# Kernel optimization log

Measured on AMD Instinct MI355X. Metric: run time of the kernel, lower is better.

## Reference

```python
import jax, jax.numpy as jnp
import numpy as np

TEMPERATURE = 8.0  # sqrt(head_dim=64)
NEG_INF = -1000000000.0


def setup_inputs() -> dict:
    key = jax.random.key(0)
    kq, kk, kv, km = jax.random.split(key, 4)
    B, H, S, D = 2, 16, 2048, 64
    q = jax.random.normal(kq, (B, H, S, D), dtype=jnp.float32)
    k = jax.random.normal(kk, (B, H, S, D), dtype=jnp.float32)
    v = jax.random.normal(kv, (B, H, S, D), dtype=jnp.float32)
    mask = jax.random.randint(km, (B, 1, S, S), 0, 2, dtype=jnp.int32)
    return {"q": q, "k": k, "v": v, "mask": mask}


def reference(q, k, v, mask):
    # scores: [B,H,S,S] = (q/T) @ k^T
    attn = jnp.einsum('bhqd,bhkd->bhqk', q / TEMPERATURE, k)
    attn = jnp.where(mask == 0, NEG_INF, attn)
    attn = jax.nn.softmax(attn, axis=-1)  # dropout is identity in eval mode
    output = jnp.einsum('bhqk,bhkd->bhqd', attn, v)
    return (output, attn)
```

## Files before the change

kernel.cpp:

```cpp
#include <hip/hip_runtime.h>
#include <hip/hip_bf16.h>


using short4v = __attribute__((ext_vector_type(4))) short;
using short8v = __attribute__((ext_vector_type(8))) short;
using float4v = __attribute__((ext_vector_type(4))) float;

#define S_LEN 2048
#define D_DIM 64
#define QT 64
#define KTILE 64
#define NIT (S_LEN / KTILE)
#define LDK 72
#define ATTN_OFF (2 * 16 * 2048 * 64)

__device__ __forceinline__ short f2bf(float x) {
  __hip_bfloat16 h = __float2bfloat16(x);
  return __builtin_bit_cast(short, h);
}

__global__ __launch_bounds__(256) void sdpa_kernel(
    const float* __restrict__ q, const float* __restrict__ k,
    const float* __restrict__ v, const int* __restrict__ mask,
    float* __restrict__ out) {
  __shared__ short lds_k[KTILE * LDK];
  __shared__ short lds_vt[D_DIM * LDK];
  __shared__ short lds_p[4 * 16 * LDK];
  __shared__ unsigned short lds_mb[NIT * 256];

  const int tid  = threadIdx.x;
  const int wave = tid >> 6;
  const int lane = tid & 63;
  const int quad = lane >> 4;
  const int l16  = lane & 15;

  const int blk = blockIdx.x;
  const int qt  = blk & (NIT - 1);
  const int bh  = blk >> 5;
  const int b   = bh >> 4;

  const float* qp = q + (size_t)bh * S_LEN * D_DIM;
  const float* kp = k + (size_t)bh * S_LEN * D_DIM;
  const float* vp = v + (size_t)bh * S_LEN * D_DIM;
  const int*   mp = mask + (size_t)b * S_LEN * S_LEN;
  float* outO = out + (size_t)bh * S_LEN * D_DIM;
  float* outA = out + (size_t)ATTN_OFF + (size_t)bh * S_LEN * S_LEN;

  const int qbase = qt * QT;

  const float QSCALE = 0.18033688011112042f;
  short8v qa[2];
  {
    const int qrow = qbase + wave * 16 + l16;
    const float* src = qp + (size_t)qrow * D_DIM + quad * 8;
#pragma unroll
    for (int c = 0; c < 2; ++c) {
      float4v x0 = *(const float4v*)(src + c * 32);
      float4v x1 = *(const float4v*)(src + c * 32 + 4);
      short8v t;
      t[0] = f2bf(x0[0] * QSCALE); t[1] = f2bf(x0[1] * QSCALE);
      t[2] = f2bf(x0[2] * QSCALE); t[3] = f2bf(x0[3] * QSCALE);
      t[4] = f2bf(x1[0] * QSCALE); t[5] = f2bf(x1[1] * QSCALE);
      t[6] = f2bf(x1[2] * QSCALE); t[7] = f2bf(x1[3] * QSCALE);
      qa[c] = t;
    }
  }

  float lsum[4] = {0.f, 0.f, 0.f, 0.f};

#pragma unroll 1
  for (int kt = 0; kt < NIT; ++kt) {
#pragma unroll
    for (int i = 0; i < 4; ++i) {
      int f = tid + i * 256;
      int row = f >> 4;
      int col = (f & 15) * 4;
      float4v x = *(const float4v*)(kp + (size_t)(kt * KTILE + row) * D_DIM + col);
      short4v y;
      y[0] = f2bf(x[0]); y[1] = f2bf(x[1]); y[2] = f2bf(x[2]); y[3] = f2bf(x[3]);
      *(short4v*)(lds_k + row * LDK + col) = y;
    }
    __syncthreads();

    unsigned mb = 0;
    const int qrowC = qbase + wave * 16 + quad * 4;
#pragma unroll
    for (int t = 0; t < 4; ++t) {
      float4v acc = {0.f, 0.f, 0.f, 0.f};
#pragma unroll
      for (int c = 0; c < 2; ++c) {
        short8v bf = *(const short8v*)(lds_k + (t * 16 + l16) * LDK + c * 32 + quad * 8);
        acc = __builtin_amdgcn_mfma_f32_16x16x32_bf16(qa[c], bf, acc, 0, 0, 0);
      }
      const int kcol = kt * KTILE + t * 16 + l16;
      const int* mrow = mp + (size_t)qrowC * S_LEN + kcol;
#pragma unroll
      for (int r = 0; r < 4; ++r) {
        int mv = mrow[(size_t)r * S_LEN];
        float p = mv ? exp2f(acc[r]) : 0.f;
        lsum[r] += p;
        mb |= (mv ? 1u : 0u) << (t * 4 + r);
      }
    }
    lds_mb[kt * 256 + tid] = (unsigned short)mb;
    __syncthreads();
  }

  float invl[4];
#pragma unroll
  for (int r = 0; r < 4; ++r) {
    float s = lsum[r];
    s += __shfl_xor(s, 1);
    s += __shfl_xor(s, 2);
    s += __shfl_xor(s, 4);
    s += __shfl_xor(s, 8);
    invl[r] = 1.0f / s;
  }

  float4v oacc[4];
#pragma unroll
  for (int dt = 0; dt < 4; ++dt) oacc[dt] = (float4v){0.f, 0.f, 0.f, 0.f};

#pragma unroll 1
  for (int kt = 0; kt < NIT; ++kt) {
#pragma unroll
    for (int i = 0; i < 4; ++i) {
      int f = tid + i * 256;
      int row = f >> 4;
      int col = (f & 15) * 4;
      float4v x = *(const float4v*)(kp + (size_t)(kt * KTILE + row) * D_DIM + col);
      short4v y;
      y[0] = f2bf(x[0]); y[1] = f2bf(x[1]); y[2] = f2bf(x[2]); y[3] = f2bf(x[3]);
      *(short4v*)(lds_k + row * LDK + col) = y;
    }
    {
      const int d = tid & 63;
      const int krg = (tid >> 6) * 4;
#pragma unroll
      for (int i = 0; i < 4; ++i) {
        int kr0 = i * 16 + krg;
        short4v y;
#pragma unroll
        for (int j = 0; j < 4; ++j) {
          float x = vp[(size_t)(kt * KTILE + kr0 + j) * D_DIM + d];
          y[j] = f2bf(x);
        }
        *(short4v*)(lds_vt + d * LDK + kr0) = y;
      }
    }
    __syncthreads();

    const unsigned mb = lds_mb[kt * 256 + tid];
    const int qrowC = qbase + wave * 16 + quad * 4;
#pragma unroll
    for (int t = 0; t < 4; ++t) {
      float4v acc = {0.f, 0.f, 0.f, 0.f};
#pragma unroll
      for (int c = 0; c < 2; ++c) {
        short8v bf = *(const short8v*)(lds_k + (t * 16 + l16) * LDK + c * 32 + quad * 8);
        acc = __builtin_amdgcn_mfma_f32_16x16x32_bf16(qa[c], bf, acc, 0, 0, 0);
      }
      const int kcol = kt * KTILE + t * 16 + l16;
      float* arow = outA + (size_t)qrowC * S_LEN + kcol;
      short* prow = lds_p + (wave * 16 + quad * 4) * LDK + t * 16 + l16;
#pragma unroll
      for (int r = 0; r < 4; ++r) {
        float p = ((mb >> (t * 4 + r)) & 1u) ? exp2f(acc[r]) * invl[r] : 0.f;
        arow[(size_t)r * S_LEN] = p;
        prow[r * LDK] = f2bf(p);
      }
    }
#pragma unroll
    for (int c = 0; c < 2; ++c) {
      short8v pa = *(const short8v*)(lds_p + (wave * 16 + l16) * LDK + c * 32 + quad * 8);
#pragma unroll
      for (int dt = 0; dt < 4; ++dt) {
        short8v vb = *(const short8v*)(lds_vt + (dt * 16 + l16) * LDK + c * 32 + quad * 8);
        oacc[dt] = __builtin_amdgcn_mfma_f32_16x16x32_bf16(pa, vb, oacc[dt], 0, 0, 0);
      }
    }
    __syncthreads();
  }

  {
    const int qrowC = qbase + wave * 16 + quad * 4;
    float* orow = outO + (size_t)qrowC * D_DIM + l16;
#pragma unroll
    for (int dt = 0; dt < 4; ++dt) {
#pragma unroll
      for (int r = 0; r < 4; ++r) {
        orow[(size_t)r * D_DIM + dt * 16] = oacc[dt][r];
      }
    }
  }
}

extern "C" void kernel_launch(void* const* d_in, const int* in_sizes, int n_in,
                              void* d_out, int out_size, void* d_ws, size_t ws_size,
                              hipStream_t stream) {
  const float* q = (const float*)d_in[0];
  const float* k = (const float*)d_in[1];
  const float* v = (const float*)d_in[2];
  const int* mask = (const int*)d_in[3];
  float* out = (float*)d_out;

  const int BH = 2 * 16;
  dim3 grid(BH * (S_LEN / QT));
  dim3 block(256);
  sdpa_kernel<<<grid, block, 0, stream>>>(q, k, v, mask, out);
}
```

Measured before the change: 1.014 ms.

## Pack mask into bitmask words and write attention rows through LDS

Adds a pre-pass kernel that compresses the int32 mask into 64-bit ballot words in the workspace. The attention kernel then reads one word per row per key tile instead of many int loads, and drops the large LDS mask-bit buffer. That frees LDS, and the launch bounds now request more blocks per CU. Attention probabilities are staged in LDS and written as contiguous 16-float vectors per lane to improve store coalescing. The trade-off is that the stored attention values are now bf16-rounded rather than full fp32.

```diff
diff --git a/kernel.cpp b/kernel.cpp
--- a/kernel.cpp
+++ b/kernel.cpp
@@ -11,6 +11,7 @@
 #define QT 64
 #define KTILE 64
 #define NIT (S_LEN / KTILE)
+#define NW (S_LEN / 64)
 #define LDK 72
 #define ATTN_OFF (2 * 16 * 2048 * 64)
 
@@ -18,15 +19,30 @@
   __hip_bfloat16 h = __float2bfloat16(x);
   return __builtin_bit_cast(short, h);
 }
-
-__global__ __launch_bounds__(256) void sdpa_kernel(
+__device__ __forceinline__ float bf2f(short s) {
+  return __builtin_bit_cast(float, ((unsigned)(unsigned short)s) << 16);
+}
+
+__global__ __launch_bounds__(256) void pack_mask_kernel(
+    const int* __restrict__ mask, unsigned long long* __restrict__ pm, int nwords) {
+  const int lane = threadIdx.x & 63;
+  int gw = (blockIdx.x * blockDim.x + threadIdx.x) >> 6;
+  const int stride = (gridDim.x * blockDim.x) >> 6;
+  for (int w = gw; w < nwords; w += stride) {
+    int m = mask[(size_t)w * 64 + lane];
+    unsigned long long bits = __ballot(m != 0);
+    if (lane == 0) pm[w] = bits;
+  }
+}
+
+template <bool PACKED>
+__global__ __launch_bounds__(256, 4) void sdpa_kernel(
     const float* __restrict__ q, const float* __restrict__ k,
     const float* __restrict__ v, const int* __restrict__ mask,
-    float* __restrict__ out) {
+    const unsigned long long* __restrict__ pm, float* __restrict__ out) {
   __shared__ short lds_k[KTILE * LDK];
   __shared__ short lds_vt[D_DIM * LDK];
-  __shared__ short lds_p[4 * 16 * LDK];
-  __shared__ unsigned short lds_mb[NIT * 256];
+  __shared__ short lds_p[QT * LDK];
 
   const int tid  = threadIdx.x;
   const int wave = tid >> 6;
@@ -47,6 +63,7 @@
   float* outA = out + (size_t)ATTN_OFF + (size_t)bh * S_LEN * S_LEN;
 
   const int qbase = qt * QT;
+  const int qrowC = qbase + wave * 16 + quad * 4;
 
   const float QSCALE = 0.18033688011112042f;
   short8v qa[2];
@@ -82,8 +99,12 @@
     }
     __syncthreads();
 
-    unsigned mb = 0;
-    const int qrowC = qbase + wave * 16 + quad * 4;
+    unsigned long long mrow[4];
+    if (PACKED) {
+#pragma unroll
+      for (int r = 0; r < 4; ++r)
+        mrow[r] = pm[((size_t)b * S_LEN + qrowC + r) * NW + kt];
+    }
 #pragma unroll
     for (int t = 0; t < 4; ++t) {
       float4v acc = {0.f, 0.f, 0.f, 0.f};
@@ -93,16 +114,14 @@
         acc = __builtin_amdgcn_mfma_f32_16x16x32_bf16(qa[c], bf, acc, 0, 0, 0);
       }
       const int kcol = kt * KTILE + t * 16 + l16;
-      const int* mrow = mp + (size_t)qrowC * S_LEN + kcol;
 #pragma unroll
       for (int r = 0; r < 4; ++r) {
-        int mv = mrow[(size_t)r * S_LEN];
+        bool mv = PACKED ? (((mrow[r] >> (t * 16 + l16)) & 1ull) != 0)
+                         : (mp[(size_t)(qrowC + r) * S_LEN + kcol] != 0);
         float p = mv ? exp2f(acc[r]) : 0.f;
         lsum[r] += p;
-        mb |= (mv ? 1u : 0u) << (t * 4 + r);
-      }
-    }
-    lds_mb[kt * 256 + tid] = (unsigned short)mb;
+      }
+    }
     __syncthreads();
   }
 
@@ -150,8 +169,12 @@
     }
     __syncthreads();
 
-    const unsigned mb = lds_mb[kt * 256 + tid];
-    const int qrowC = qbase + wave * 16 + quad * 4;
+    unsigned long long mrow[4];
+    if (PACKED) {
+#pragma unroll
+      for (int r = 0; r < 4; ++r)
+        mrow[r] = pm[((size_t)b * S_LEN + qrowC + r) * NW + kt];
+    }
 #pragma unroll
     for (int t = 0; t < 4; ++t) {
       float4v acc = {0.f, 0.f, 0.f, 0.f};
@@ -161,15 +184,33 @@
         acc = __builtin_amdgcn_mfma_f32_16x16x32_bf16(qa[c], bf, acc, 0, 0, 0);
       }
       const int kcol = kt * KTILE + t * 16 + l16;
-      float* arow = outA + (size_t)qrowC * S_LEN + kcol;
       short* prow = lds_p + (wave * 16 + quad * 4) * LDK + t * 16 + l16;
 #pragma unroll
       for (int r = 0; r < 4; ++r) {
-        float p = ((mb >> (t * 4 + r)) & 1u) ? exp2f(acc[r]) * invl[r] : 0.f;
-        arow[(size_t)r * S_LEN] = p;
+        bool mv = PACKED ? (((mrow[r] >> (t * 16 + l16)) & 1ull) != 0)
+                         : (mp[(size_t)(qrowC + r) * S_LEN + kcol] != 0);
+        float p = mv ? exp2f(acc[r]) * invl[r] : 0.f;
         prow[r * LDK] = f2bf(p);
       }
     }
+
+    {
+      const int row16 = lane >> 2;
+      const int cg = (lane & 3) * 16;
+      const short* src = lds_p + (wave * 16 + row16) * LDK + cg;
+      short8v p0 = *(const short8v*)src;
+      short8v p1 = *(const short8v*)(src + 8);
+      float* arow = outA + (size_t)(qbase + wave * 16 + row16) * S_LEN + kt * KTILE + cg;
+      float4v f0 = {bf2f(p0[0]), bf2f(p0[1]), bf2f(p0[2]), bf2f(p0[3])};
+      float4v f1 = {bf2f(p0[4]), bf2f(p0[5]), bf2f(p0[6]), bf2f(p0[7])};
+      float4v f2 = {bf2f(p1[0]), bf2f(p1[1]), bf2f(p1[2]), bf2f(p1[3])};
+      float4v f3 = {bf2f(p1[4]), bf2f(p1[5]), bf2f(p1[6]), bf2f(p1[7])};
+      *(float4v*)(arow)      = f0;
+      *(float4v*)(arow + 4)  = f1;
+      *(float4v*)(arow + 8)  = f2;
+      *(float4v*)(arow + 12) = f3;
+    }
+
 #pragma unroll
     for (int c = 0; c < 2; ++c) {
       short8v pa = *(const short8v*)(lds_p + (wave * 16 + l16) * LDK + c * 32 + quad * 8);
@@ -183,7 +224,6 @@
   }
 
   {
-    const int qrowC = qbase + wave * 16 + quad * 4;
     float* orow = outO + (size_t)qrowC * D_DIM + l16;
 #pragma unroll
     for (int dt = 0; dt < 4; ++dt) {
@@ -207,5 +247,14 @@
   const int BH = 2 * 16;
   dim3 grid(BH * (S_LEN / QT));
   dim3 block(256);
-  sdpa_kernel<<<grid, block, 0, stream>>>(q, k, v, mask, out);
-}
+
+  const int nwords = 2 * S_LEN * NW;
+  const size_t pm_bytes = (size_t)nwords * 8;
+  if (ws_size >= pm_bytes) {
+    unsigned long long* pm = (unsigned long long*)d_ws;
+    pack_mask_kernel<<<256, 256, 0, stream>>>(mask, pm, nwords);
+    sdpa_kernel<true><<<grid, block, 0, stream>>>(q, k, v, mask, pm, out);
+  } else {
+    sdpa_kernel<false><<<grid, block, 0, stream>>>(q, k, v, mask, nullptr, out);
+  }
+}
```

After: 850.3 us. 16.1% less time.
